# Kernel optimization log

Measured on AMD Instinct MI355X. Metric: run time of the kernel, lower is better.

The kernel has to match this reference:

```python
import jax, jax.numpy as jnp
import numpy as np

H, C = 8, 128          # heads, per-head channels
HC = H * C             # 1024
N = 8192               # nodes
E = 98304              # edges (before self-loops)
G = 64                 # graphs
IN = 128               # in_dim
NTYPE = 32
NFAM = 64
TE = 16                # type_emb dim
L = 4                  # layers
EPS = 1e-5
SLOPE = 0.2


def setup_inputs() -> dict:
    key = jax.random.key(0)
    ks = jax.random.split(key, 32)
    g = lambda k, s, sc: jax.random.normal(k, s, dtype=jnp.float32) * sc
    inp = {}
    inp["x"] = jax.random.normal(ks[0], (N, IN), jnp.float32)
    inp["edge"] = jax.random.randint(ks[1], (2, E), 0, N)
    inp["batch"] = jnp.sort(jax.random.randint(ks[2], (N,), 0, G))
    inp["y_type"] = jax.random.randint(ks[3], (G,), 0, NTYPE)
    # layer 0 (in_dim=128 -> 1024)
    inp["Wl0"] = g(ks[4], (IN, HC), 1.0 / np.sqrt(IN))
    inp["bl0"] = jnp.zeros((HC,), jnp.float32)
    inp["Wr0"] = g(ks[5], (IN, HC), 1.0 / np.sqrt(IN))
    inp["br0"] = jnp.zeros((HC,), jnp.float32)
    inp["att0"] = g(ks[6], (H, C), 1.0 / np.sqrt(C))
    inp["b0"] = jnp.zeros((HC,), jnp.float32)
    # layers 1..3 stacked (1024 -> 1024)
    inp["Wl"] = g(ks[7], (L - 1, HC, HC), 1.0 / np.sqrt(HC))
    inp["bl"] = jnp.zeros((L - 1, HC), jnp.float32)
    inp["Wr"] = g(ks[8], (L - 1, HC, HC), 1.0 / np.sqrt(HC))
    inp["br"] = jnp.zeros((L - 1, HC), jnp.float32)
    inp["att"] = g(ks[9], (L - 1, H, C), 1.0 / np.sqrt(C))
    inp["b"] = jnp.zeros((L - 1, HC), jnp.float32)
    # LayerNorm params per layer
    inp["ln_g"] = jnp.ones((L, HC), jnp.float32)
    inp["ln_b"] = jnp.zeros((L, HC), jnp.float32)
    # heads
    inp["Temb"] = g(ks[10], (NTYPE, TE), 1.0)
    inp["W_fam"] = g(ks[11], (HC + TE, NFAM), 1.0 / np.sqrt(HC + TE))
    inp["b_fam"] = jnp.zeros((NFAM,), jnp.float32)
    inp["W_type"] = g(ks[12], (HC + TE, NTYPE), 1.0 / np.sqrt(HC + TE))
    inp["b_type"] = jnp.zeros((NTYPE,), jnp.float32)
    return inp


def _gatv2(h, src, dst, Wl, bl, Wr, br, att, bias):
    # GATv2Conv (PyG semantics, eval mode, self-loops already in src/dst)
    xl = (h @ Wl + bl).reshape(N, H, C)   # source projection
    xr = (h @ Wr + br).reshape(N, H, C)   # target projection
    m = jax.nn.leaky_relu(xl[src] + xr[dst], SLOPE)          # [E+N, H, C]
    logits = jnp.einsum('ehc,hc->eh', m, att)                # [E+N, H]
    lmax = jax.ops.segment_max(logits, dst, num_segments=N)  # [N, H]
    e = jnp.exp(logits - lmax[dst])
    denom = jax.ops.segment_sum(e, dst, num_segments=N)
    alpha = e / denom[dst]                                   # [E+N, H]
    out = jax.ops.segment_sum(xl[src] * alpha[:, :, None], dst, num_segments=N)
    return out.reshape(N, HC) + bias


def _ln(z, gamma, beta):
    mu = jnp.mean(z, axis=-1, keepdims=True)
    var = jnp.var(z, axis=-1, keepdims=True)
    return (z - mu) * jax.lax.rsqrt(var + EPS) * gamma + beta


def reference(x, edge, batch, y_type, Wl0, bl0, Wr0, br0, att0, b0,
              Wl, bl, Wr, br, att, b, ln_g, ln_b, Temb,
              W_fam, b_fam, W_type, b_type):
    loops = jnp.arange(N, dtype=edge.dtype)
    src = jnp.concatenate([edge[0], loops])
    dst = jnp.concatenate([edge[1], loops])
    # layer 0: no residual (in_dim != hidden*heads)
    h = _ln(jax.nn.relu(_gatv2(x, src, dst, Wl0, bl0, Wr0, br0, att0, b0)), ln_g[0], ln_b[0])
    for i in range(L - 1):
        z = jax.nn.relu(_gatv2(h, src, dst, Wl[i], bl[i], Wr[i], br[i], att[i], b[i]))
        h = _ln(z, ln_g[i + 1], ln_b[i + 1]) + h
    # global mean pool
    sums = jax.ops.segment_sum(h, batch, num_segments=G)
    cnts = jax.ops.segment_sum(jnp.ones((N,), h.dtype), batch, num_segments=G)
    gfeat = sums / jnp.maximum(cnts, 1.0)[:, None]
    gfeat = jnp.concatenate([gfeat, Temb[y_type]], axis=1)    # [G, HC+TE]
    return (gfeat @ W_fam + b_fam, gfeat @ W_type + b_type)
```

## Files before the change

kernel.cpp:

```cpp
#include <hip/hip_runtime.h>
#include <hip/hip_bf16.h>
#include <type_traits>
#include <utility>

#define NNODE 8192
#define EE    98304
#define ETOT  (EE + NNODE)
#define GG    64
#define HC    1024
#define NCAT  2048
#define MAXDEG 128
#define SLOPE 0.2f

typedef unsigned short u16;

__device__ __forceinline__ float bf2f(u16 u){
  union { unsigned int i; float f; } v; v.i = ((unsigned int)u) << 16; return v.f;
}
__device__ __forceinline__ u16 f2bf(float f){
  unsigned int x = __float_as_uint(f);
  unsigned int r = (x + 0x7fffu + ((x >> 16) & 1u)) >> 16;
  return (u16)r;
}
__device__ __forceinline__ float lo16(unsigned int u){ return __uint_as_float(u << 16); }
__device__ __forceinline__ float hi16(unsigned int u){ return __uint_as_float(u & 0xffff0000u); }

__device__ __forceinline__ float rdf(const void* p, int i, int fl){
  return fl ? ((const float*)p)[i] : bf2f(((const u16*)p)[i]);
}

__device__ __forceinline__ void unpack8(const uint4& u, float* f){
  f[0]=lo16(u.x); f[1]=hi16(u.x); f[2]=lo16(u.y); f[3]=hi16(u.y);
  f[4]=lo16(u.z); f[5]=hi16(u.z); f[6]=lo16(u.w); f[7]=hi16(u.w);
}

template <typename T>
__device__ __forceinline__ auto nt_store_impl(const T& v, T* p, int)
    -> decltype(__builtin_nontemporal_store(v, p), void()) {
  __builtin_nontemporal_store(v, p);
}
template <typename T>
__device__ __forceinline__ void nt_store_impl(const T& v, T* p, long) { *p = v; }
template <typename T>
__device__ __forceinline__ void nt_store(const T& v, T* p) { nt_store_impl(v, p, 0); }

__global__ void sniff_kernel(const unsigned int* __restrict__ x, int* __restrict__ flag){
  __shared__ int cnt;
  if (threadIdx.x == 0) cnt = 0;
  __syncthreads();
  const unsigned int w = x[threadIdx.x];
  const int e = (w >> 23) & 0xFF;
  if (e >= 97 && e <= 158) atomicAdd(&cnt, 1);
  __syncthreads();
  if (threadIdx.x == 0) *flag = (cnt > 128) ? 1 : 0;
}

__global__ void convert_kernel(const void* __restrict__ src, u16* __restrict__ dst,
                               int n, const int* __restrict__ flag){
  const int i = blockIdx.x * 256 + threadIdx.x;
  if (i >= n) return;
  dst[i] = (*flag) ? f2bf(((const float*)src)[i]) : ((const u16*)src)[i];
}

typedef float  f32x4 __attribute__((ext_vector_type(4)));
typedef __bf16 b16x8 __attribute__((ext_vector_type(8)));
typedef short  s16x8 __attribute__((ext_vector_type(8)));

template <typename V, typename = void> struct MfmaOk : std::false_type {};
template <typename V>
struct MfmaOk<V, std::void_t<decltype(__builtin_amdgcn_mfma_f32_16x16x32_bf16(
    std::declval<V>(), std::declval<V>(), std::declval<f32x4>(), 0, 0, 0))>>
    : std::true_type {};

using frag_t = std::conditional_t<MfmaOk<b16x8>::value, b16x8, s16x8>;

__device__ __forceinline__ f32x4 mfma16(frag_t a, frag_t b, f32x4 c){
  return __builtin_amdgcn_mfma_f32_16x16x32_bf16(a, b, c, 0, 0, 0);
}

__device__ __forceinline__ void gl_lds16(const u16* g, u16* l){
  __builtin_amdgcn_global_load_lds(
      (const __attribute__((address_space(1))) unsigned int*)(const void*)g,
      (__attribute__((address_space(3))) unsigned int*)(void*)l, 16, 0, 0);
}

__global__ __launch_bounds__(256) void gemm_bt(
    const u16* __restrict__ A, const u16* __restrict__ Bt,
    const float* __restrict__ bias, u16* __restrict__ C, int K)
{
  __shared__ __align__(16) u16 smem[16384];
  u16* lA = smem;
  u16* lB = smem + 8192;
  const int tid = threadIdx.x, lane = tid & 63;
  const int wid = tid >> 6;
  const int lin = blockIdx.x;
  const int by = (lin & 7) * 8 + ((lin >> 3) & 7);
  const int bx = lin >> 6;
  const int m0 = by * 128, n0 = bx * 128;
  const int wm = (wid >> 1) * 64, wn = (wid & 1) * 64;

  f32x4 acc[4][4];
  #pragma unroll
  for (int i = 0; i < 4; i++)
    #pragma unroll
    for (int j = 0; j < 4; j++)
      #pragma unroll
      for (int r = 0; r < 4; r++) acc[i][j][r] = 0.f;

  const int r8 = lane >> 3, sl = lane & 7;
  const int gch = sl ^ r8;
  const u16* ga = A  + (size_t)(m0 + wid * 32 + r8) * K + gch * 8;
  const u16* gb = Bt + (size_t)(n0 + wid * 32 + r8) * K + gch * 8;

  const int fr = lane & 15, q = lane >> 4;

  for (int k0 = 0; k0 < K; k0 += 64) {
    __syncthreads();
    #pragma unroll
    for (int t = 0; t < 4; t++) {
      gl_lds16(ga + (size_t)t * 8 * K + k0, lA + (wid * 32 + t * 8) * 64);
      gl_lds16(gb + (size_t)t * 8 * K + k0, lB + (wid * 32 + t * 8) * 64);
    }
    __syncthreads();
    #pragma unroll
    for (int ks = 0; ks < 2; ks++) {
      const int cb = ks * 4 + q;
      frag_t af[4], bf[4];
      #pragma unroll
      for (int i = 0; i < 4; i++) {
        int r = wm + i * 16 + fr;
        af[i] = *(const frag_t*)(lA + r * 64 + (cb ^ (r & 7)) * 8);
      }
      #pragma unroll
      for (int j = 0; j < 4; j++) {
        int r = wn + j * 16 + fr;
        bf[j] = *(const frag_t*)(lB + r * 64 + (cb ^ (r & 7)) * 8);
      }
      #pragma unroll
      for (int i = 0; i < 4; i++)
        #pragma unroll
        for (int j = 0; j < 4; j++)
          acc[i][j] = mfma16(af[i], bf[j], acc[i][j]);
    }
  }

  __syncthreads();
  u16* sc = smem + wid * 2304;
  float bj[4];
  #pragma unroll
  for (int j = 0; j < 4; j++) bj[j] = bias[n0 + wn + j * 16 + fr];
  const int rb8 = lane >> 3, cc = lane & 7;
  #pragma unroll
  for (int p = 0; p < 2; p++) {
    #pragma unroll
    for (int ii = 0; ii < 2; ii++) {
      const int i = 2 * p + ii;
      #pragma unroll
      for (int j = 0; j < 4; j++)
        #pragma unroll
        for (int r = 0; r < 4; r++)
          sc[(ii * 16 + q * 4 + r) * 72 + j * 16 + fr] = f2bf(acc[i][j][r] + bj[j]);
    }
    #pragma unroll
    for (int t = 0; t < 4; t++) {
      const int lrow = t * 8 + rb8;
      const uint4 v = *(const uint4*)(sc + lrow * 72 + cc * 8);
      nt_store(v, (uint4*)(C + (size_t)(m0 + wm + p * 32 + lrow) * NCAT
                             + (n0 + wn + cc * 8)));
    }
  }
}

__global__ void transpose_all(const void* __restrict__ Wl0, const void* __restrict__ Wr0,
                              const void* __restrict__ Wl, const void* __restrict__ Wr,
                              u16* __restrict__ bt0, u16* __restrict__ btL,
                              const int* __restrict__ flag){
  __shared__ u16 tile[32][33];
  const int z = blockIdx.z;
  int K, off; const void* in; u16* out;
  if (z < 2){
    if (blockIdx.y >= 4) return;
    K = 128; off = 0;
    in = z ? Wr0 : Wl0;
    out = bt0 + (size_t)z * 1024 * 128;
  } else {
    const int l = (z - 2) >> 1, part = (z - 2) & 1;
    K = 1024; off = l * 1024 * 1024;
    in = part ? Wr : Wl;
    out = btL + (size_t)l * 2048 * 1024 + (size_t)part * 1024 * 1024;
  }
  const int fl = *flag;
  const int n0 = blockIdx.x * 32, k0 = blockIdx.y * 32;
  const int x = threadIdx.x, y = threadIdx.y;
  for (int i = y; i < 32; i += 8){
    const int idx = off + (k0 + i) * 1024 + n0 + x;
    tile[i][x] = fl ? f2bf(((const float*)in)[idx]) : ((const u16*)in)[idx];
  }
  __syncthreads();
  for (int i = y; i < 32; i += 8) out[(size_t)(n0 + i) * K + k0 + x] = tile[x][i];
}

__global__ void prep_misc(
    const void* __restrict__ bl0, const void* __restrict__ br0,
    const void* __restrict__ bl, const void* __restrict__ br,
    const void* __restrict__ wfam, const void* __restrict__ bfam,
    const void* __restrict__ wtyp, const void* __restrict__ btyp,
    const void* __restrict__ att0, const void* __restrict__ attL,
    const void* __restrict__ b0, const void* __restrict__ bgL,
    const void* __restrict__ lng, const void* __restrict__ lnb,
    float* __restrict__ ball, u16* __restrict__ wT,
    float* __restrict__ bhead, float* __restrict__ nparm,
    const int* __restrict__ flag)
{
  int i = blockIdx.x * 256 + threadIdx.x;
  const int fl = *flag;
  if (i < 8192){
    const int l = i >> 11, j = i & 2047;
    float v;
    if (l == 0) v = (j < 1024) ? rdf(bl0, j, fl) : rdf(br0, j - 1024, fl);
    else        v = (j < 1024) ? rdf(bl, (l - 1) * 1024 + j, fl)
                               : rdf(br, (l - 1) * 1024 + (j - 1024), fl);
    ball[i] = v;
    return;
  }
  i -= 8192;
  if (i < 96 * 1040){
    const int j = i / 1040, k = i - j * 1040;
    const float v = (j < 64) ? rdf(wfam, k * 64 + j, fl)
                             : rdf(wtyp, k * 32 + (j - 64), fl);
    wT[j * 1040 + k] = f2bf(v);
    return;
  }
  i -= 96 * 1040;
  if (i < 96){
    bhead[i] = (i < 64) ? rdf(bfam, i, fl) : rdf(btyp, i - 64, fl);
    return;
  }
  i -= 96;
  if (i < 4 * 4 * 1024){
    const int l = i >> 12, a = (i >> 10) & 3, c = i & 1023;
    float v;
    if (a == 0)      v = (l == 0) ? rdf(att0, c, fl) : rdf(attL, (l - 1) * 1024 + c, fl);
    else if (a == 1) v = (l == 0) ? rdf(b0, c, fl)   : rdf(bgL, (l - 1) * 1024 + c, fl);
    else if (a == 2) v = rdf(lng, l * 1024 + c, fl);
    else             v = rdf(lnb, l * 1024 + c, fl);
    nparm[i] = v;
  }
}

__global__ void count_kernel(const int* __restrict__ edge, int* __restrict__ cnt){
  const int i = blockIdx.x * 256 + threadIdx.x;
  if (i >= ETOT) return;
  const int d = (i < EE) ? edge[EE + i] : (i - EE);
  atomicAdd(&cnt[d], 1);
}

__global__ __launch_bounds__(1024) void scan_kernel(const int* __restrict__ cnt,
    int* __restrict__ rowptr, int* __restrict__ fillpos){
  __shared__ int sc[1024];
  const int t = threadIdx.x;
  int loc[8]; int s = 0;
  #pragma unroll
  for (int i = 0; i < 8; i++){ loc[i] = cnt[t * 8 + i]; s += loc[i]; }
  sc[t] = s; __syncthreads();
  for (int off = 1; off < 1024; off <<= 1){
    int v = (t >= off) ? sc[t - off] : 0;
    __syncthreads();
    sc[t] += v;
    __syncthreads();
  }
  int base = sc[t] - s;
  #pragma unroll
  for (int i = 0; i < 8; i++){ rowptr[t * 8 + i] = base; fillpos[t * 8 + i] = base; base += loc[i]; }
  if (t == 1023) rowptr[NNODE] = base;
}

__global__ void fill_kernel(const int* __restrict__ edge, int* __restrict__ fillpos,
                            int* __restrict__ csr){
  const int i = blockIdx.x * 256 + threadIdx.x;
  if (i >= ETOT) return;
  int s, d;
  if (i < EE){ s = edge[i]; d = edge[EE + i]; } else { s = d = i - EE; }
  const int p = atomicAdd(&fillpos[d], 1);
  csr[p] = s;
}

__global__ __launch_bounds__(256) void node_kernel(
    const u16* __restrict__ xlr, const u16* __restrict__ hprev,
    const int* __restrict__ rowptr, const int* __restrict__ csr,
    const float* __restrict__ parm, u16* __restrict__ hout)
{
  const int tid = threadIdx.x, lane = tid & 63, wid = tid >> 6;
  const int half = tid >> 7, t = tid & 127;
  const int d = blockIdx.x * 2 + half;
  const int rs = rowptr[d];
  int deg = rowptr[d + 1] - rs;
  if (deg > MAXDEG) deg = MAXDEG;

  __shared__ int   s_src[2][MAXDEG];
  __shared__ float s_red[8];

  for (int i = t; i < deg; i += 128) s_src[half][i] = csr[rs + i];

  const int c0 = t * 8;
  float xr[8], at[8];
  unpack8(*(const uint4*)(xlr + (size_t)d * NCAT + HC + c0), xr);
  {
    const float4 u0 = *(const float4*)(parm + c0);
    const float4 u1 = *(const float4*)(parm + c0 + 4);
    at[0]=u0.x; at[1]=u0.y; at[2]=u0.z; at[3]=u0.w;
    at[4]=u1.x; at[5]=u1.y; at[6]=u1.z; at[7]=u1.w;
  }
  __syncthreads();

  float lA = 0.f, lB = 0.f;
  float accA[8], accB[8];
  #pragma unroll
  for (int i = 0; i < 8; i++){ accA[i] = 0.f; accB[i] = 0.f; }

  const int e2 = deg & ~1;
  for (int ei = 0; ei < e2; ei += 2){
    const int sa = s_src[half][ei], sb = s_src[half][ei + 1];
    const uint4 ua = *(const uint4*)(xlr + (size_t)sa * NCAT + c0);
    const uint4 ub = *(const uint4*)(xlr + (size_t)sb * NCAT + c0);
    float xa[8], xb[8];
    unpack8(ua, xa); unpack8(ub, xb);
    float pa = 0.f, pb = 0.f;
    #pragma unroll
    for (int i = 0; i < 8; i++){
      float va = xa[i] + xr[i]; va = (va > 0.f) ? va : SLOPE * va; pa += va * at[i];
      float vb = xb[i] + xr[i]; vb = (vb > 0.f) ? vb : SLOPE * vb; pb += vb * at[i];
    }
    pa += __shfl_xor(pa, 1); pb += __shfl_xor(pb, 1);
    pa += __shfl_xor(pa, 2); pb += __shfl_xor(pb, 2);
    pa += __shfl_xor(pa, 4); pb += __shfl_xor(pb, 4);
    pa += __shfl_xor(pa, 8); pb += __shfl_xor(pb, 8);
    const float ea = __expf(pa), eb = __expf(pb);
    lA += ea; lB += eb;
    #pragma unroll
    for (int i = 0; i < 8; i++){ accA[i] += ea * xa[i]; accB[i] += eb * xb[i]; }
  }
  if (deg & 1){
    const int sa = s_src[half][deg - 1];
    float xa[8];
    unpack8(*(const uint4*)(xlr + (size_t)sa * NCAT + c0), xa);
    float pa = 0.f;
    #pragma unroll
    for (int i = 0; i < 8; i++){
      float va = xa[i] + xr[i]; va = (va > 0.f) ? va : SLOPE * va; pa += va * at[i];
    }
    pa += __shfl_xor(pa, 1); pa += __shfl_xor(pa, 2);
    pa += __shfl_xor(pa, 4); pa += __shfl_xor(pa, 8);
    const float ea = __expf(pa);
    lA += ea;
    #pragma unroll
    for (int i = 0; i < 8; i++) accA[i] += ea * xa[i];
  }

  const float inv = 1.f / (lA + lB);
  float z[8];
  #pragma unroll
  for (int i = 0; i < 8; i++) z[i] = (accA[i] + accB[i]) * inv;

  {
    const float4 g0 = *(const float4*)(parm + 1024 + c0);
    const float4 g1 = *(const float4*)(parm + 1024 + c0 + 4);
    const float gb[8] = {g0.x, g0.y, g0.z, g0.w, g1.x, g1.y, g1.z, g1.w};
    #pragma unroll
    for (int i = 0; i < 8; i++) z[i] = fmaxf(z[i] + gb[i], 0.f);
  }
  float sum = 0.f, sq = 0.f;
  #pragma unroll
  for (int i = 0; i < 8; i++){ sum += z[i]; sq += z[i] * z[i]; }
  #pragma unroll
  for (int off = 1; off < 64; off <<= 1){ sum += __shfl_xor(sum, off); sq += __shfl_xor(sq, off); }
  if (lane == 0){ s_red[wid] = sum; s_red[4 + wid] = sq; }
  __syncthreads();
  const float tsum = s_red[half * 2] + s_red[half * 2 + 1];
  const float tsq  = s_red[4 + half * 2] + s_red[4 + half * 2 + 1];
  const float mean = tsum * (1.f / 1024.f);
  const float var  = tsq * (1.f / 1024.f) - mean * mean;
  const float rstd = rsqrtf(var + 1e-5f);
  float y[8];
  {
    const float4 g0 = *(const float4*)(parm + 2048 + c0);
    const float4 g1 = *(const float4*)(parm + 2048 + c0 + 4);
    const float4 h0 = *(const float4*)(parm + 3072 + c0);
    const float4 h1 = *(const float4*)(parm + 3072 + c0 + 4);
    const float gg[8] = {g0.x, g0.y, g0.z, g0.w, g1.x, g1.y, g1.z, g1.w};
    const float bb[8] = {h0.x, h0.y, h0.z, h0.w, h1.x, h1.y, h1.z, h1.w};
    #pragma unroll
    for (int i = 0; i < 8; i++) y[i] = (z[i] - mean) * rstd * gg[i] + bb[i];
  }
  if (hprev){
    float hp[8];
    unpack8(*(const uint4*)(hprev + (size_t)d * HC + c0), hp);
    #pragma unroll
    for (int i = 0; i < 8; i++) y[i] += hp[i];
  }
  uint4 o;
  o.x = (unsigned)f2bf(y[0]) | ((unsigned)f2bf(y[1]) << 16);
  o.y = (unsigned)f2bf(y[2]) | ((unsigned)f2bf(y[3]) << 16);
  o.z = (unsigned)f2bf(y[4]) | ((unsigned)f2bf(y[5]) << 16);
  o.w = (unsigned)f2bf(y[6]) | ((unsigned)f2bf(y[7]) << 16);
  *(uint4*)(hout + (size_t)d * HC + c0) = o;
}

__device__ __forceinline__ int lbound(const int* a, int n, int v){
  int lo = 0, hi = n;
  while (lo < hi){ int mid = (lo + hi) >> 1; if (a[mid] < v) lo = mid + 1; else hi = mid; }
  return lo;
}

__global__ __launch_bounds__(256) void pool_kernel(const u16* __restrict__ hfin,
    const int* __restrict__ batch, const int* __restrict__ ytype,
    const void* __restrict__ temb, const int* __restrict__ flag,
    float* __restrict__ gfeat)
{
  const int g = blockIdx.x, t = threadIdx.x;
  const int s = lbound(batch, NNODE, g);
  const int e = lbound(batch, NNODE, g + 1);
  float a0 = 0, a1 = 0, a2 = 0, a3 = 0;
  for (int n = s; n < e; n++){
    const uint2 u = *(const uint2*)(hfin + (size_t)n * HC + t * 4);
    a0 += lo16(u.x); a1 += hi16(u.x); a2 += lo16(u.y); a3 += hi16(u.y);
  }
  const float inv = 1.f / fmaxf((float)(e - s), 1.f);
  float* gp = gfeat + g * 1040 + t * 4;
  gp[0] = a0 * inv; gp[1] = a1 * inv; gp[2] = a2 * inv; gp[3] = a3 * inv;
  if (t < 16) gfeat[g * 1040 + 1024 + t] = rdf(temb, ytype[g] * 16 + t, *flag);
}

__global__ __launch_bounds__(128) void head_kernel(const float* __restrict__ gfeat,
    const u16* __restrict__ wT, const float* __restrict__ bhead,
    const int* __restrict__ flag, void* __restrict__ outp)
{
  const int g = blockIdx.x, t = threadIdx.x;
  __shared__ float gf[1040];
  for (int i = t; i < 1040; i += 128) gf[i] = gfeat[g * 1040 + i];
  __syncthreads();
  if (t >= 96) return;
  float acc = bhead[t];
  const u16* wp = wT + t * 1040;
  #pragma unroll 4
  for (int k = 0; k < 1040; k += 8){
    const uint4 u = *(const uint4*)(wp + k);
    acc += gf[k+0]*lo16(u.x) + gf[k+1]*hi16(u.x)
         + gf[k+2]*lo16(u.y) + gf[k+3]*hi16(u.y)
         + gf[k+4]*lo16(u.z) + gf[k+5]*hi16(u.z)
         + gf[k+6]*lo16(u.w) + gf[k+7]*hi16(u.w);
  }
  const int fl = *flag;
  const int idx = (t < 64) ? (g * 64 + t) : (4096 + g * 32 + (t - 64));
  if (fl) ((float*)outp)[idx] = acc;
  else    ((u16*)outp)[idx] = f2bf(acc);
}

extern "C" void kernel_launch(void* const* d_in, const int* in_sizes, int n_in,
                              void* d_out, int out_size, void* d_ws, size_t ws_size,
                              hipStream_t stream)
{
  (void)in_sizes; (void)n_in; (void)out_size; (void)ws_size;
  const void* x    = d_in[0];
  const int* edge  = (const int*)d_in[1];
  const int* batch = (const int*)d_in[2];
  const int* ytyp  = (const int*)d_in[3];
  const void* Wl0  = d_in[4];
  const void* bl0  = d_in[5];
  const void* Wr0  = d_in[6];
  const void* br0  = d_in[7];
  const void* att0 = d_in[8];
  const void* b0   = d_in[9];
  const void* Wl   = d_in[10];
  const void* bl   = d_in[11];
  const void* Wr   = d_in[12];
  const void* br   = d_in[13];
  const void* att  = d_in[14];
  const void* bg   = d_in[15];
  const void* lng  = d_in[16];
  const void* lnb  = d_in[17];
  const void* temb = d_in[18];
  const void* wfam = d_in[19];
  const void* bfam = d_in[20];
  const void* wtyp = d_in[21];
  const void* btyp = d_in[22];

  char* w = (char*)d_ws;
  auto alloc = [&](size_t b){ char* p = w; w += (b + 255) & ~(size_t)255; return (void*)p; };
  u16* bt0 = (u16*)alloc((size_t)2048 * 128 * 2);
  u16* btL = (u16*)alloc((size_t)3 * 2048 * 1024 * 2);
  float* ball = (float*)alloc((size_t)4 * 2048 * 4);
  u16* xbf = (u16*)alloc((size_t)NNODE * 128 * 2);
  u16* xlr = (u16*)alloc((size_t)NNODE * NCAT * 2);
  u16* hA  = (u16*)alloc((size_t)NNODE * HC * 2);
  u16* hB  = (u16*)alloc((size_t)NNODE * HC * 2);
  int* cnt     = (int*)alloc((size_t)NNODE * 4);
  int* rowptr  = (int*)alloc((size_t)(NNODE + 1) * 4);
  int* fillpos = (int*)alloc((size_t)NNODE * 4);
  int* csr     = (int*)alloc((size_t)ETOT * 4);
  float* gfeat = (float*)alloc((size_t)GG * 1040 * 4);
  u16* wT      = (u16*)alloc((size_t)96 * 1040 * 2);
  float* bhead = (float*)alloc((size_t)96 * 4);
  float* nparm = (float*)alloc((size_t)4 * 4 * 1024 * 4);
  int* flag    = (int*)alloc(256);

  sniff_kernel<<<1, 256, 0, stream>>>((const unsigned int*)x, flag);
  convert_kernel<<<(NNODE * 128 + 255) / 256, 256, 0, stream>>>(x, xbf, NNODE * 128, flag);

  (void)hipMemsetAsync(cnt, 0, NNODE * 4, stream);
  count_kernel<<<(ETOT + 255) / 256, 256, 0, stream>>>(edge, cnt);
  scan_kernel<<<1, 1024, 0, stream>>>(cnt, rowptr, fillpos);
  fill_kernel<<<(ETOT + 255) / 256, 256, 0, stream>>>(edge, fillpos, csr);

  const int prep_n = 8192 + 96 * 1040 + 96 + 4 * 4 * 1024;
  prep_misc<<<(prep_n + 255) / 256, 256, 0, stream>>>(
      bl0, br0, bl, br, wfam, bfam, wtyp, btyp,
      att0, att, b0, bg, lng, lnb,
      ball, wT, bhead, nparm, flag);
  transpose_all<<<dim3(32, 32, 8), dim3(32, 8), 0, stream>>>(
      Wl0, Wr0, Wl, Wr, bt0, btL, flag);

  gemm_bt<<<1024, 256, 0, stream>>>(xbf, bt0, ball, xlr, 128);
  node_kernel<<<NNODE / 2, 256, 0, stream>>>(xlr, nullptr, rowptr, csr, nparm, hA);

  u16* hcur = hA; u16* hnext = hB;
  for (int l = 1; l < 4; l++){
    gemm_bt<<<1024, 256, 0, stream>>>(hcur, btL + (size_t)(l - 1) * 2048 * 1024,
                                      ball + l * 2048, xlr, 1024);
    node_kernel<<<NNODE / 2, 256, 0, stream>>>(xlr, hcur, rowptr, csr,
                                               nparm + l * 4096, hnext);
    u16* t2 = hcur; hcur = hnext; hnext = t2;
  }

  pool_kernel<<<GG, 256, 0, stream>>>(hcur, batch, ytyp, temb, flag, gfeat);
  head_kernel<<<GG, 128, 0, stream>>>(gfeat, wT, bhead, flag, (void*)d_out);
}
```

Baseline: 536.7 us.

## Drop dtype sniffing, bucket edges into fixed-capacity slots, fuse pool and head

```diff
diff --git a/kernel.cpp b/kernel.cpp
--- a/kernel.cpp
+++ b/kernel.cpp
@@ -9,14 +9,11 @@
 #define GG    64
 #define HC    1024
 #define NCAT  2048
-#define MAXDEG 128
+#define DEGCAP 64
 #define SLOPE 0.2f
 
 typedef unsigned short u16;
 
-__device__ __forceinline__ float bf2f(u16 u){
-  union { unsigned int i; float f; } v; v.i = ((unsigned int)u) << 16; return v.f;
-}
 __device__ __forceinline__ u16 f2bf(float f){
   unsigned int x = __float_as_uint(f);
   unsigned int r = (x + 0x7fffu + ((x >> 16) & 1u)) >> 16;
@@ -25,10 +22,6 @@
 __device__ __forceinline__ float lo16(unsigned int u){ return __uint_as_float(u << 16); }
 __device__ __forceinline__ float hi16(unsigned int u){ return __uint_as_float(u & 0xffff0000u); }
 
-__device__ __forceinline__ float rdf(const void* p, int i, int fl){
-  return fl ? ((const float*)p)[i] : bf2f(((const u16*)p)[i]);
-}
-
 __device__ __forceinline__ void unpack8(const uint4& u, float* f){
   f[0]=lo16(u.x); f[1]=hi16(u.x); f[2]=lo16(u.y); f[3]=hi16(u.y);
   f[4]=lo16(u.z); f[5]=hi16(u.z); f[6]=lo16(u.w); f[7]=hi16(u.w);
@@ -44,22 +37,11 @@
 template <typename T>
 __device__ __forceinline__ void nt_store(const T& v, T* p) { nt_store_impl(v, p, 0); }
 
-__global__ void sniff_kernel(const unsigned int* __restrict__ x, int* __restrict__ flag){
-  __shared__ int cnt;
-  if (threadIdx.x == 0) cnt = 0;
-  __syncthreads();
-  const unsigned int w = x[threadIdx.x];
-  const int e = (w >> 23) & 0xFF;
-  if (e >= 97 && e <= 158) atomicAdd(&cnt, 1);
-  __syncthreads();
-  if (threadIdx.x == 0) *flag = (cnt > 128) ? 1 : 0;
-}
-
-__global__ void convert_kernel(const void* __restrict__ src, u16* __restrict__ dst,
-                               int n, const int* __restrict__ flag){
+__global__ void convert_kernel(const float* __restrict__ src, u16* __restrict__ dst,
+                               int* __restrict__ cnt){
   const int i = blockIdx.x * 256 + threadIdx.x;
-  if (i >= n) return;
-  dst[i] = (*flag) ? f2bf(((const float*)src)[i]) : ((const u16*)src)[i];
+  if (i < NNODE * 128) dst[i] = f2bf(src[i]);
+  if (i < NNODE) cnt[i] = 0;
 }
 
 typedef float  f32x4 __attribute__((ext_vector_type(4)));
@@ -88,7 +70,7 @@
     const u16* __restrict__ A, const u16* __restrict__ Bt,
     const float* __restrict__ bias, u16* __restrict__ C, int K)
 {
-  __shared__ __align__(16) u16 smem[16384];
+  __shared__ __align__(16) u16 smem[4 * 64 * 72];
   u16* lA = smem;
   u16* lB = smem + 8192;
   const int tid = threadIdx.x, lane = tid & 63;
@@ -145,39 +127,31 @@
   }
 
   __syncthreads();
-  u16* sc = smem + wid * 2304;
-  float bj[4];
-  #pragma unroll
-  for (int j = 0; j < 4; j++) bj[j] = bias[n0 + wn + j * 16 + fr];
+  u16* sc = smem + wid * (64 * 72);
+  #pragma unroll
+  for (int i = 0; i < 4; i++)
+    #pragma unroll
+    for (int j = 0; j < 4; j++) {
+      const float bj = bias[n0 + wn + j * 16 + fr];
+      #pragma unroll
+      for (int r = 0; r < 4; r++)
+        sc[(i * 16 + q * 4 + r) * 72 + j * 16 + fr] = f2bf(acc[i][j][r] + bj);
+    }
   const int rb8 = lane >> 3, cc = lane & 7;
   #pragma unroll
-  for (int p = 0; p < 2; p++) {
-    #pragma unroll
-    for (int ii = 0; ii < 2; ii++) {
-      const int i = 2 * p + ii;
-      #pragma unroll
-      for (int j = 0; j < 4; j++)
-        #pragma unroll
-        for (int r = 0; r < 4; r++)
-          sc[(ii * 16 + q * 4 + r) * 72 + j * 16 + fr] = f2bf(acc[i][j][r] + bj[j]);
-    }
-    #pragma unroll
-    for (int t = 0; t < 4; t++) {
-      const int lrow = t * 8 + rb8;
-      const uint4 v = *(const uint4*)(sc + lrow * 72 + cc * 8);
-      nt_store(v, (uint4*)(C + (size_t)(m0 + wm + p * 32 + lrow) * NCAT
-                             + (n0 + wn + cc * 8)));
-    }
-  }
-}
-
-__global__ void transpose_all(const void* __restrict__ Wl0, const void* __restrict__ Wr0,
-                              const void* __restrict__ Wl, const void* __restrict__ Wr,
-                              u16* __restrict__ bt0, u16* __restrict__ btL,
-                              const int* __restrict__ flag){
+  for (int t = 0; t < 8; t++) {
+    const int row = t * 8 + rb8;
+    const uint4 v = *(const uint4*)(sc + row * 72 + cc * 8);
+    nt_store(v, (uint4*)(C + (size_t)(m0 + wm + row) * NCAT + (n0 + wn + cc * 8)));
+  }
+}
+
+__global__ void transpose_all(const float* __restrict__ Wl0, const float* __restrict__ Wr0,
+                              const float* __restrict__ Wl, const float* __restrict__ Wr,
+                              u16* __restrict__ bt0, u16* __restrict__ btL){
   __shared__ u16 tile[32][33];
   const int z = blockIdx.z;
-  int K, off; const void* in; u16* out;
+  int K, off; const float* in; u16* out;
   if (z < 2){
     if (blockIdx.y >= 4) return;
     K = 128; off = 0;
@@ -189,118 +163,83 @@
     in = part ? Wr : Wl;
     out = btL + (size_t)l * 2048 * 1024 + (size_t)part * 1024 * 1024;
   }
-  const int fl = *flag;
   const int n0 = blockIdx.x * 32, k0 = blockIdx.y * 32;
   const int x = threadIdx.x, y = threadIdx.y;
-  for (int i = y; i < 32; i += 8){
-    const int idx = off + (k0 + i) * 1024 + n0 + x;
-    tile[i][x] = fl ? f2bf(((const float*)in)[idx]) : ((const u16*)in)[idx];
-  }
+  for (int i = y; i < 32; i += 8)
+    tile[i][x] = f2bf(in[off + (k0 + i) * 1024 + n0 + x]);
   __syncthreads();
   for (int i = y; i < 32; i += 8) out[(size_t)(n0 + i) * K + k0 + x] = tile[x][i];
 }
 
 __global__ void prep_misc(
-    const void* __restrict__ bl0, const void* __restrict__ br0,
-    const void* __restrict__ bl, const void* __restrict__ br,
-    const void* __restrict__ wfam, const void* __restrict__ bfam,
-    const void* __restrict__ wtyp, const void* __restrict__ btyp,
-    const void* __restrict__ att0, const void* __restrict__ attL,
-    const void* __restrict__ b0, const void* __restrict__ bgL,
-    const void* __restrict__ lng, const void* __restrict__ lnb,
+    const float* __restrict__ bl0, const float* __restrict__ br0,
+    const float* __restrict__ bl, const float* __restrict__ br,
+    const float* __restrict__ wfam, const float* __restrict__ bfam,
+    const float* __restrict__ wtyp, const float* __restrict__ btyp,
+    const float* __restrict__ att0, const float* __restrict__ attL,
+    const float* __restrict__ b0, const float* __restrict__ bgL,
+    const float* __restrict__ lng, const float* __restrict__ lnb,
     float* __restrict__ ball, u16* __restrict__ wT,
-    float* __restrict__ bhead, float* __restrict__ nparm,
-    const int* __restrict__ flag)
+    float* __restrict__ bhead, float* __restrict__ nparm)
 {
   int i = blockIdx.x * 256 + threadIdx.x;
-  const int fl = *flag;
   if (i < 8192){
     const int l = i >> 11, j = i & 2047;
     float v;
-    if (l == 0) v = (j < 1024) ? rdf(bl0, j, fl) : rdf(br0, j - 1024, fl);
-    else        v = (j < 1024) ? rdf(bl, (l - 1) * 1024 + j, fl)
-                               : rdf(br, (l - 1) * 1024 + (j - 1024), fl);
+    if (l == 0) v = (j < 1024) ? bl0[j] : br0[j - 1024];
+    else        v = (j < 1024) ? bl[(l - 1) * 1024 + j] : br[(l - 1) * 1024 + (j - 1024)];
     ball[i] = v;
     return;
   }
   i -= 8192;
   if (i < 96 * 1040){
     const int j = i / 1040, k = i - j * 1040;
-    const float v = (j < 64) ? rdf(wfam, k * 64 + j, fl)
-                             : rdf(wtyp, k * 32 + (j - 64), fl);
+    const float v = (j < 64) ? wfam[k * 64 + j] : wtyp[k * 32 + (j - 64)];
     wT[j * 1040 + k] = f2bf(v);
     return;
   }
   i -= 96 * 1040;
   if (i < 96){
-    bhead[i] = (i < 64) ? rdf(bfam, i, fl) : rdf(btyp, i - 64, fl);
+    bhead[i] = (i < 64) ? bfam[i] : btyp[i - 64];
     return;
   }
   i -= 96;
   if (i < 4 * 4 * 1024){
     const int l = i >> 12, a = (i >> 10) & 3, c = i & 1023;
     float v;
-    if (a == 0)      v = (l == 0) ? rdf(att0, c, fl) : rdf(attL, (l - 1) * 1024 + c, fl);
-    else if (a == 1) v = (l == 0) ? rdf(b0, c, fl)   : rdf(bgL, (l - 1) * 1024 + c, fl);
-    else if (a == 2) v = rdf(lng, l * 1024 + c, fl);
-    else             v = rdf(lnb, l * 1024 + c, fl);
+    if (a == 0)      v = (l == 0) ? att0[c] : attL[(l - 1) * 1024 + c];
+    else if (a == 1) v = (l == 0) ? b0[c]   : bgL[(l - 1) * 1024 + c];
+    else if (a == 2) v = lng[l * 1024 + c];
+    else             v = lnb[l * 1024 + c];
     nparm[i] = v;
   }
 }
 
-__global__ void count_kernel(const int* __restrict__ edge, int* __restrict__ cnt){
-  const int i = blockIdx.x * 256 + threadIdx.x;
-  if (i >= ETOT) return;
-  const int d = (i < EE) ? edge[EE + i] : (i - EE);
-  atomicAdd(&cnt[d], 1);
-}
-
-__global__ __launch_bounds__(1024) void scan_kernel(const int* __restrict__ cnt,
-    int* __restrict__ rowptr, int* __restrict__ fillpos){
-  __shared__ int sc[1024];
-  const int t = threadIdx.x;
-  int loc[8]; int s = 0;
-  #pragma unroll
-  for (int i = 0; i < 8; i++){ loc[i] = cnt[t * 8 + i]; s += loc[i]; }
-  sc[t] = s; __syncthreads();
-  for (int off = 1; off < 1024; off <<= 1){
-    int v = (t >= off) ? sc[t - off] : 0;
-    __syncthreads();
-    sc[t] += v;
-    __syncthreads();
-  }
-  int base = sc[t] - s;
-  #pragma unroll
-  for (int i = 0; i < 8; i++){ rowptr[t * 8 + i] = base; fillpos[t * 8 + i] = base; base += loc[i]; }
-  if (t == 1023) rowptr[NNODE] = base;
-}
-
-__global__ void fill_kernel(const int* __restrict__ edge, int* __restrict__ fillpos,
-                            int* __restrict__ csr){
+__global__ void bucket_kernel(const int* __restrict__ edge, int* __restrict__ cnt,
+                              int* __restrict__ csr){
   const int i = blockIdx.x * 256 + threadIdx.x;
   if (i >= ETOT) return;
   int s, d;
   if (i < EE){ s = edge[i]; d = edge[EE + i]; } else { s = d = i - EE; }
-  const int p = atomicAdd(&fillpos[d], 1);
-  csr[p] = s;
+  const int p = atomicAdd(&cnt[d], 1);
+  if (p < DEGCAP) csr[d * DEGCAP + p] = s;
 }
 
 __global__ __launch_bounds__(256) void node_kernel(
     const u16* __restrict__ xlr, const u16* __restrict__ hprev,
-    const int* __restrict__ rowptr, const int* __restrict__ csr,
+    const int* __restrict__ cnt, const int* __restrict__ csr,
     const float* __restrict__ parm, u16* __restrict__ hout)
 {
   const int tid = threadIdx.x, lane = tid & 63, wid = tid >> 6;
   const int half = tid >> 7, t = tid & 127;
   const int d = blockIdx.x * 2 + half;
-  const int rs = rowptr[d];
-  int deg = rowptr[d + 1] - rs;
-  if (deg > MAXDEG) deg = MAXDEG;
-
-  __shared__ int   s_src[2][MAXDEG];
+  int deg = cnt[d];
+  if (deg > DEGCAP) deg = DEGCAP;
+
+  __shared__ int   s_src[2][DEGCAP];
   __shared__ float s_red[8];
 
-  for (int i = t; i < deg; i += 128) s_src[half][i] = csr[rs + i];
+  for (int i = t; i < deg; i += 128) s_src[half][i] = csr[d * DEGCAP + i];
 
   const int c0 = t * 8;
   float xr[8], at[8];
@@ -412,12 +351,13 @@
   return lo;
 }
 
-__global__ __launch_bounds__(256) void pool_kernel(const u16* __restrict__ hfin,
+__global__ __launch_bounds__(256) void poolhead_kernel(const u16* __restrict__ hfin,
     const int* __restrict__ batch, const int* __restrict__ ytype,
-    const void* __restrict__ temb, const int* __restrict__ flag,
-    float* __restrict__ gfeat)
+    const float* __restrict__ temb, const u16* __restrict__ wT,
+    const float* __restrict__ bhead, float* __restrict__ outp)
 {
   const int g = blockIdx.x, t = threadIdx.x;
+  __shared__ float gf[1040];
   const int s = lbound(batch, NNODE, g);
   const int e = lbound(batch, NNODE, g + 1);
   float a0 = 0, a1 = 0, a2 = 0, a3 = 0;
@@ -426,18 +366,9 @@
     a0 += lo16(u.x); a1 += hi16(u.x); a2 += lo16(u.y); a3 += hi16(u.y);
   }
   const float inv = 1.f / fmaxf((float)(e - s), 1.f);
-  float* gp = gfeat + g * 1040 + t * 4;
-  gp[0] = a0 * inv; gp[1] = a1 * inv; gp[2] = a2 * inv; gp[3] = a3 * inv;
-  if (t < 16) gfeat[g * 1040 + 1024 + t] = rdf(temb, ytype[g] * 16 + t, *flag);
-}
-
-__global__ __launch_bounds__(128) void head_kernel(const float* __restrict__ gfeat,
-    const u16* __restrict__ wT, const float* __restrict__ bhead,
-    const int* __restrict__ flag, void* __restrict__ outp)
-{
-  const int g = blockIdx.x, t = threadIdx.x;
-  __shared__ float gf[1040];
-  for (int i = t; i < 1040; i += 128) gf[i] = gfeat[g * 1040 + i];
+  gf[t * 4 + 0] = a0 * inv; gf[t * 4 + 1] = a1 * inv;
+  gf[t * 4 + 2] = a2 * inv; gf[t * 4 + 3] = a3 * inv;
+  if (t < 16) gf[1024 + t] = temb[ytype[g] * 16 + t];
   __syncthreads();
   if (t >= 96) return;
   float acc = bhead[t];
@@ -450,10 +381,8 @@
          + gf[k+4]*lo16(u.z) + gf[k+5]*hi16(u.z)
          + gf[k+6]*lo16(u.w) + gf[k+7]*hi16(u.w);
   }
-  const int fl = *flag;
   const int idx = (t < 64) ? (g * 64 + t) : (4096 + g * 32 + (t - 64));
-  if (fl) ((float*)outp)[idx] = acc;
-  else    ((u16*)outp)[idx] = f2bf(acc);
+  outp[idx] = acc;
 }
 
 extern "C" void kernel_launch(void* const* d_in, const int* in_sizes, int n_in,
@@ -461,29 +390,29 @@
                               hipStream_t stream)
 {
   (void)in_sizes; (void)n_in; (void)out_size; (void)ws_size;
-  const void* x    = d_in[0];
-  const int* edge  = (const int*)d_in[1];
-  const int* batch = (const int*)d_in[2];
-  const int* ytyp  = (const int*)d_in[3];
-  const void* Wl0  = d_in[4];
-  const void* bl0  = d_in[5];
-  const void* Wr0  = d_in[6];
-  const void* br0  = d_in[7];
-  const void* att0 = d_in[8];
-  const void* b0   = d_in[9];
-  const void* Wl   = d_in[10];
-  const void* bl   = d_in[11];
-  const void* Wr   = d_in[12];
-  const void* br   = d_in[13];
-  const void* att  = d_in[14];
-  const void* bg   = d_in[15];
-  const void* lng  = d_in[16];
-  const void* lnb  = d_in[17];
-  const void* temb = d_in[18];
-  const void* wfam = d_in[19];
-  const void* bfam = d_in[20];
-  const void* wtyp = d_in[21];
-  const void* btyp = d_in[22];
+  const float* x    = (const float*)d_in[0];
+  const int* edge   = (const int*)d_in[1];
+  const int* batch  = (const int*)d_in[2];
+  const int* ytyp   = (const int*)d_in[3];
+  const float* Wl0  = (const float*)d_in[4];
+  const float* bl0  = (const float*)d_in[5];
+  const float* Wr0  = (const float*)d_in[6];
+  const float* br0  = (const float*)d_in[7];
+  const float* att0 = (const float*)d_in[8];
+  const float* b0   = (const float*)d_in[9];
+  const float* Wl   = (const float*)d_in[10];
+  const float* bl   = (const float*)d_in[11];
+  const float* Wr   = (const float*)d_in[12];
+  const float* br   = (const float*)d_in[13];
+  const float* att  = (const float*)d_in[14];
+  const float* bg   = (const float*)d_in[15];
+  const float* lng  = (const float*)d_in[16];
+  const float* lnb  = (const float*)d_in[17];
+  const float* temb = (const float*)d_in[18];
+  const float* wfam = (const float*)d_in[19];
+  const float* bfam = (const float*)d_in[20];
+  const float* wtyp = (const float*)d_in[21];
+  const float* btyp = (const float*)d_in[22];
 
   char* w = (char*)d_ws;
   auto alloc = [&](size_t b){ char* p = w; w += (b + 255) & ~(size_t)255; return (void*)p; };
@@ -494,44 +423,35 @@
   u16* xlr = (u16*)alloc((size_t)NNODE * NCAT * 2);
   u16* hA  = (u16*)alloc((size_t)NNODE * HC * 2);
   u16* hB  = (u16*)alloc((size_t)NNODE * HC * 2);
-  int* cnt     = (int*)alloc((size_t)NNODE * 4);
-  int* rowptr  = (int*)alloc((size_t)(NNODE + 1) * 4);
-  int* fillpos = (int*)alloc((size_t)NNODE * 4);
-  int* csr     = (int*)alloc((size_t)ETOT * 4);
-  float* gfeat = (float*)alloc((size_t)GG * 1040 * 4);
+  int* cnt = (int*)alloc((size_t)NNODE * 4);
+  int* csr = (int*)alloc((size_t)NNODE * DEGCAP * 4);
   u16* wT      = (u16*)alloc((size_t)96 * 1040 * 2);
   float* bhead = (float*)alloc((size_t)96 * 4);
   float* nparm = (float*)alloc((size_t)4 * 4 * 1024 * 4);
-  int* flag    = (int*)alloc(256);
-
-  sniff_kernel<<<1, 256, 0, stream>>>((const unsigned int*)x, flag);
-  convert_kernel<<<(NNODE * 128 + 255) / 256, 256, 0, stream>>>(x, xbf, NNODE * 128, flag);
-
-  (void)hipMemsetAsync(cnt, 0, NNODE * 4, stream);
-  count_kernel<<<(ETOT + 255) / 256, 256, 0, stream>>>(edge, cnt);
-  scan_kernel<<<1, 1024, 0, stream>>>(cnt, rowptr, fillpos);
-  fill_kernel<<<(ETOT + 255) / 256, 256, 0, stream>>>(edge, fillpos, csr);
+
+  convert_kernel<<<(NNODE * 128 + 255) / 256, 256, 0, stream>>>(x, xbf, cnt);
+  bucket_kernel<<<(ETOT + 255) / 256, 256, 0, stream>>>(edge, cnt, csr);
 
   const int prep_n = 8192 + 96 * 1040 + 96 + 4 * 4 * 1024;
   prep_misc<<<(prep_n + 255) / 256, 256, 0, stream>>>(
       bl0, br0, bl, br, wfam, bfam, wtyp, btyp,
       att0, att, b0, bg, lng, lnb,
-      ball, wT, bhead, nparm, flag);
+      ball, wT, bhead, nparm);
   transpose_all<<<dim3(32, 32, 8), dim3(32, 8), 0, stream>>>(
-      Wl0, Wr0, Wl, Wr, bt0, btL, flag);
+      Wl0, Wr0, Wl, Wr, bt0, btL);
 
   gemm_bt<<<1024, 256, 0, stream>>>(xbf, bt0, ball, xlr, 128);
-  node_kernel<<<NNODE / 2, 256, 0, stream>>>(xlr, nullptr, rowptr, csr, nparm, hA);
+  node_kernel<<<NNODE / 2, 256, 0, stream>>>(xlr, nullptr, cnt, csr, nparm, hA);
 
   u16* hcur = hA; u16* hnext = hB;
   for (int l = 1; l < 4; l++){
     gemm_bt<<<1024, 256, 0, stream>>>(hcur, btL + (size_t)(l - 1) * 2048 * 1024,
                                       ball + l * 2048, xlr, 1024);
-    node_kernel<<<NNODE / 2, 256, 0, stream>>>(xlr, hcur, rowptr, csr,
+    node_kernel<<<NNODE / 2, 256, 0, stream>>>(xlr, hcur, cnt, csr,
                                                nparm + l * 4096, hnext);
     u16* t2 = hcur; hcur = hnext; hnext = t2;
   }
 
-  pool_kernel<<<GG, 256, 0, stream>>>(hcur, batch, ytyp, temb, flag, gfeat);
-  head_kernel<<<GG, 128, 0, stream>>>(gfeat, wT, bhead, flag, (void*)d_out);
-}
+  poolhead_kernel<<<GG, 256, 0, stream>>>(hcur, batch, ytyp, temb, wT, bhead,
+                                          (float*)d_out);
+}
```

New measurement: 496.2 us. -7.5%, faster.
